# Performance work log

Measured on AMD Instinct MI355X. Metric: run time of the kernel, lower is better.

The kernel has to match this reference:

```python
import jax, jax.numpy as jnp
import numpy as np

NUM_NODES = 10000
NUM_EDGES = 640000
IN_CH = 128
HID = 128
OUT_CH = 1


def setup_inputs() -> dict:
    key = jax.random.key(0)
    ks = jax.random.split(key, 12)
    x = jax.random.normal(ks[0], (NUM_NODES, IN_CH), dtype=jnp.float32)
    edge_index = jax.random.randint(ks[1], (2, NUM_EDGES), 0, NUM_NODES, dtype=jnp.int64)
    edge_weight = jax.random.uniform(ks[2], (NUM_EDGES,), dtype=jnp.float32)
    s1 = 1.0 / np.sqrt(IN_CH)
    s2 = 1.0 / np.sqrt(HID)
    W1 = jax.random.uniform(ks[3], (HID, IN_CH), minval=-s1, maxval=s1, dtype=jnp.float32)
    b1 = jnp.zeros((HID,), dtype=jnp.float32)
    W2 = jax.random.uniform(ks[4], (HID, HID), minval=-s2, maxval=s2, dtype=jnp.float32)
    b2 = jnp.zeros((HID,), dtype=jnp.float32)
    sc = 1.0 / np.sqrt(HID * 3)
    conv_w = jax.random.uniform(ks[5], (HID, HID, 3), minval=-sc, maxval=sc, dtype=jnp.float32)
    conv_b = jax.random.uniform(ks[6], (HID,), minval=-sc, maxval=sc, dtype=jnp.float32)
    fc_w = jax.random.uniform(ks[7], (OUT_CH, HID), minval=-s2, maxval=s2, dtype=jnp.float32)
    fc_b = jax.random.uniform(ks[8], (OUT_CH,), minval=-s2, maxval=s2, dtype=jnp.float32)
    return {"x": x, "edge_index": edge_index, "edge_weight": edge_weight,
            "W1": W1, "b1": b1, "W2": W2, "b2": b2,
            "conv_w": conv_w, "conv_b": conv_b, "fc_w": fc_w, "fc_b": fc_b}


def _gcn_conv(x, row, col, norm, W, b):
    # PyG GCNConv: linear (no bias in lin), normalized scatter-add, then bias
    xw = x @ W.T                                   # [N, out]
    msg = xw[row] * norm[:, None]                  # gather + edge scale [E, out]
    out = jax.ops.segment_sum(msg, col, num_segments=NUM_NODES)
    return out + b


def reference(x, edge_index, edge_weight, W1, b1, W2, b2, conv_w, conv_b, fc_w, fc_b):
    # gcn_norm with self-loops (fill_value=1.0)
    loop = jnp.arange(NUM_NODES, dtype=edge_index.dtype)
    row = jnp.concatenate([edge_index[0], loop])
    col = jnp.concatenate([edge_index[1], loop])
    w = jnp.concatenate([edge_weight, jnp.ones((NUM_NODES,), dtype=edge_weight.dtype)])
    deg = jax.ops.segment_sum(w, col, num_segments=NUM_NODES)
    dinv = jnp.where(deg > 0, jax.lax.rsqrt(deg), 0.0)
    norm = dinv[row] * w * dinv[col]

    h = jax.nn.relu(_gcn_conv(x, row, col, norm, W1, b1))
    # dropout is identity in eval mode
    h = jax.nn.relu(_gcn_conv(h, row, col, norm, W2, b2))

    # temporal conv1d over node axis: [N,H] -> [1,H,N]
    hc = h.T[None, :, :]
    hc = jax.lax.conv_general_dilated(hc, conv_w, window_strides=(1,),
                                      padding='SAME',
                                      dimension_numbers=('NCH', 'OIH', 'NCH'))
    hc = hc + conv_b[None, :, None]
    h = hc[0].T                                    # [N, H]

    return (h @ fc_w.T + fc_b).squeeze()           # [N]
```

## Files before the change

kernel.cpp:

```cpp
#include <hip/hip_runtime.h>
#include <hip/hip_bf16.h>

#define N_NODES 10000
#define N_EDGES 640000
#define CH 128
#define NB 128
#define EPB (N_EDGES / NB)
#define NCHUNK 40

__global__ __launch_bounds__(256) void hist_kernel(const int* __restrict__ ei,
                                                   const float* __restrict__ ew,
                                                   int* __restrict__ hist,
                                                   float* __restrict__ dhist) {
    __shared__ int h[N_NODES];
    __shared__ float hf[N_NODES];
    int b = blockIdx.x, t = threadIdx.x;
    for (int i = t; i < N_NODES; i += 256) { h[i] = 0; hf[i] = 0.0f; }
    __syncthreads();
    int e0 = b * EPB;
    for (int i = t; i < EPB; i += 256) {
        int c = ei[N_EDGES + e0 + i];
        float w = ew[e0 + i];
        atomicAdd(&h[c], 1);
        atomicAdd(&hf[c], w);
    }
    __syncthreads();
    for (int i = t; i < N_NODES; i += 256) {
        hist[b * N_NODES + i] = h[i];
        dhist[b * N_NODES + i] = hf[i];
    }
}

__global__ __launch_bounds__(256) void reduce_kernel(const int* __restrict__ hist,
        const float* __restrict__ dhist, int* __restrict__ tot,
        float* __restrict__ dinv, int* __restrict__ csum,
        const float* __restrict__ conv_w, const float* __restrict__ conv_b,
        const float* __restrict__ fc_w, const float* __restrict__ fc_b,
        float* __restrict__ vbuf, float* __restrict__ c0) {
    int blk = blockIdx.x, t = threadIdx.x;
    if (blk == NCHUNK) {
        for (int i = t; i <= 384; i += 256) {
            if (i < 384) {
                float s = 0.0f;
                for (int o = 0; o < CH; ++o) s += fc_w[o] * conv_w[o * 384 + i];
                vbuf[i] = s;
            } else {
                float s = fc_b[0];
                for (int o = 0; o < CH; ++o) s += fc_w[o] * conv_b[o];
                *c0 = s;
            }
        }
        return;
    }
    int n = blk * 256 + t;
    int c = 0;
    if (n < N_NODES) {
        float d = 0.0f;
        #pragma unroll 4
        for (int b = 0; b < NB; ++b) {
            c += hist[b * N_NODES + n];
            d += dhist[b * N_NODES + n];
        }
        tot[n] = c;
        dinv[n] = rsqrtf(d + 1.0f);
    }
    __shared__ int wred[4];
    int lane = t & 63, wave = t >> 6;
    int s = c;
    #pragma unroll
    for (int off = 32; off > 0; off >>= 1) s += __shfl_down(s, off, 64);
    if (lane == 0) wred[wave] = s;
    __syncthreads();
    if (t == 0) csum[blk] = wred[0] + wred[1] + wred[2] + wred[3];
}

__global__ __launch_bounds__(256) void bofs_kernel(int* __restrict__ hist,
        const int* __restrict__ tot, const int* __restrict__ csum,
        int* __restrict__ offs) {
    __shared__ int lds_csum[NCHUNK];
    __shared__ int wsum[4];
    int blk = blockIdx.x, t = threadIdx.x;
    if (t < NCHUNK) lds_csum[t] = csum[t];
    __syncthreads();
    int base = 0;
    for (int i = 0; i < blk; ++i) base += lds_csum[i];
    int n = blk * 256 + t;
    int v = (n < N_NODES) ? tot[n] : 0;
    int lane = t & 63, wave = t >> 6;
    int s = v;
    #pragma unroll
    for (int off = 1; off < 64; off <<= 1) {
        int u = __shfl_up(s, off, 64);
        if (lane >= off) s += u;
    }
    if (lane == 63) wsum[wave] = s;
    __syncthreads();
    int wbase = 0;
    for (int i = 0; i < wave; ++i) wbase += wsum[i];
    if (n < N_NODES) {
        int run = base + wbase + s - v;
        offs[n] = run;
        for (int b = 0; b < NB; ++b) {
            int h = hist[b * N_NODES + n];
            hist[b * N_NODES + n] = run;
            run += h;
        }
    }
}

__global__ __launch_bounds__(256) void scatter_kernel(const int* __restrict__ ei,
        const float* __restrict__ ew, const float* __restrict__ dinv,
        const int* __restrict__ bofs, int2* __restrict__ erec) {
    __shared__ int cur[N_NODES];
    __shared__ float di[N_NODES];
    int b = blockIdx.x, t = threadIdx.x;
    for (int i = t; i < N_NODES; i += 256) {
        cur[i] = bofs[b * N_NODES + i];
        di[i] = dinv[i];
    }
    __syncthreads();
    int e0 = b * EPB;
    for (int i = t; i < EPB; i += 256) {
        int e = e0 + i;
        int r = ei[e];
        int c = ei[N_EDGES + e];
        int p = atomicAdd(&cur[c], 1);
        float v = di[r] * ew[e] * di[c];
        erec[p] = make_int2(r, __float_as_int(v));
    }
}

__global__ __launch_bounds__(256) void gemm128_kernel(const float* __restrict__ A,
                                                      const float* __restrict__ W,
                                                      float* __restrict__ out, int M) {
    __shared__ float As[32][68];
    __shared__ float Ws[32][132];
    int tid = threadIdx.x;
    int tx = tid & 31;
    int ty = tid >> 5;
    int row0 = blockIdx.x * 64;
    float acc[8][4] = {};
    for (int k0 = 0; k0 < 128; k0 += 32) {
        #pragma unroll
        for (int i = 0; i < 8; ++i) {
            int idx = tid + i * 256;
            int r = idx >> 5, k = idx & 31;
            int gr = row0 + r;
            As[k][r] = (gr < M) ? A[gr * CH + k0 + k] : 0.0f;
        }
        #pragma unroll
        for (int i = 0; i < 16; ++i) {
            int idx = tid + i * 256;
            int o = idx >> 5, k = idx & 31;
            Ws[k][o] = W[o * CH + k0 + k];
        }
        __syncthreads();
        #pragma unroll
        for (int kk = 0; kk < 32; ++kk) {
            float a[8], w[4];
            #pragma unroll
            for (int j = 0; j < 8; ++j) a[j] = As[kk][ty * 8 + j];
            #pragma unroll
            for (int c = 0; c < 4; ++c) w[c] = Ws[kk][tx * 4 + c];
            #pragma unroll
            for (int j = 0; j < 8; ++j)
                #pragma unroll
                for (int c = 0; c < 4; ++c)
                    acc[j][c] += a[j] * w[c];
        }
        __syncthreads();
    }
    #pragma unroll
    for (int j = 0; j < 8; ++j) {
        int gr = row0 + ty * 8 + j;
        if (gr < M) {
            float4 v = make_float4(acc[j][0], acc[j][1], acc[j][2], acc[j][3]);
            *reinterpret_cast<float4*>(&out[gr * CH + tx * 4]) = v;
        }
    }
}

__global__ __launch_bounds__(256) void agg_kernel(const float4* __restrict__ xw4,
        const int2* __restrict__ erec, const int* __restrict__ offs,
        const int* __restrict__ cnt, const float* __restrict__ dinv,
        const float4* __restrict__ bias4, float4* __restrict__ out4) {
    int l = threadIdx.x & 31;
    int g = threadIdx.x >> 5;
    int n = blockIdx.x * 8 + g;
    float d = dinv[n];
    float dd = d * d;
    float4 self = xw4[n * 32 + l];
    float4 acc = make_float4(dd * self.x, dd * self.y, dd * self.z, dd * self.w);
    int start = offs[n];
    int num = cnt[n];
    int i = 0;
    for (; i + 8 <= num; i += 8) {
        int2 r[8];
        #pragma unroll
        for (int j = 0; j < 8; ++j) r[j] = erec[start + i + j];
        float4 f[8];
        #pragma unroll
        for (int j = 0; j < 8; ++j) f[j] = xw4[r[j].x * 32 + l];
        #pragma unroll
        for (int j = 0; j < 8; ++j) {
            float v = __int_as_float(r[j].y);
            acc.x += v * f[j].x; acc.y += v * f[j].y;
            acc.z += v * f[j].z; acc.w += v * f[j].w;
        }
    }
    for (; i < num; ++i) {
        int2 r = erec[start + i];
        float4 f = xw4[r.x * 32 + l];
        float v = __int_as_float(r.y);
        acc.x += v * f.x; acc.y += v * f.y; acc.z += v * f.z; acc.w += v * f.w;
    }
    float4 bb = bias4[l];
    acc.x = fmaxf(acc.x + bb.x, 0.0f);
    acc.y = fmaxf(acc.y + bb.y, 0.0f);
    acc.z = fmaxf(acc.z + bb.z, 0.0f);
    acc.w = fmaxf(acc.w + bb.w, 0.0f);
    out4[n * 32 + l] = acc;
}

__global__ __launch_bounds__(128) void convfc_kernel(const float* __restrict__ h,
        const float* __restrict__ v, const float* __restrict__ c0,
        float* __restrict__ out, int N) {
    int n = blockIdx.x;
    int t = threadIdx.x;
    float p = 0.0f;
    if (n > 0)     p += h[(n - 1) * CH + t] * v[t * 3 + 0];
    p += h[n * CH + t] * v[t * 3 + 1];
    if (n < N - 1) p += h[(n + 1) * CH + t] * v[t * 3 + 2];
    #pragma unroll
    for (int off = 32; off > 0; off >>= 1) p += __shfl_down(p, off, 64);
    __shared__ float red[2];
    if ((t & 63) == 0) red[t >> 6] = p;
    __syncthreads();
    if (t == 0) out[n] = red[0] + red[1] + *c0;
}

extern "C" void kernel_launch(void* const* d_in, const int* in_sizes, int n_in,
                              void* d_out, int out_size, void* d_ws, size_t ws_size,
                              hipStream_t stream) {
    const float* x       = (const float*)d_in[0];
    const int*   ei      = (const int*)d_in[1];
    const float* ew      = (const float*)d_in[2];
    const float* W1      = (const float*)d_in[3];
    const float* b1      = (const float*)d_in[4];
    const float* W2      = (const float*)d_in[5];
    const float* b2      = (const float*)d_in[6];
    const float* conv_w  = (const float*)d_in[7];
    const float* conv_b  = (const float*)d_in[8];
    const float* fc_w    = (const float*)d_in[9];
    const float* fc_b    = (const float*)d_in[10];
    float* out = (float*)d_out;

    float* bufA   = (float*)d_ws;
    float* bufB   = bufA + N_NODES * CH;
    int2*  erec   = (int2*)(bufB + N_NODES * CH);
    int*   hist   = (int*)bufA;
    float* dhist  = (float*)erec;
    int*   tot    = (int*)(erec + N_EDGES);
    int*   offs   = tot + N_NODES;
    float* dinv   = (float*)(offs + N_NODES);
    float* vbuf   = dinv + N_NODES;
    float* c0     = vbuf + 384;
    int*   csum   = (int*)(c0 + 1);

    hist_kernel<<<NB, 256, 0, stream>>>(ei, ew, hist, dhist);
    reduce_kernel<<<NCHUNK + 1, 256, 0, stream>>>(hist, dhist, tot, dinv, csum,
                                                  conv_w, conv_b, fc_w, fc_b, vbuf, c0);
    bofs_kernel<<<NCHUNK, 256, 0, stream>>>(hist, tot, csum, offs);
    scatter_kernel<<<NB, 256, 0, stream>>>(ei, ew, dinv, hist, erec);

    const int gemm_grid = (N_NODES + 63) / 64;
    gemm128_kernel<<<gemm_grid, 256, 0, stream>>>(x, W1, bufA, N_NODES);
    agg_kernel<<<N_NODES / 8, 256, 0, stream>>>((const float4*)bufA, erec, offs, tot,
                                                dinv, (const float4*)b1, (float4*)bufB);
    gemm128_kernel<<<gemm_grid, 256, 0, stream>>>(bufB, W2, bufA, N_NODES);
    agg_kernel<<<N_NODES / 8, 256, 0, stream>>>((const float4*)bufA, erec, offs, tot,
                                                dinv, (const float4*)b2, (float4*)bufB);
    convfc_kernel<<<N_NODES, 128, 0, stream>>>(bufB, vbuf, c0, out, N_NODES);
}
```

Baseline: 229.2 us.

## Replace per-block histogram CSR build with global atomics and single-block scan

The CSR construction changes from 128 per-block LDS histograms, a reduce pass, and a per-block offset pass to global atomic counting of degrees, one 1024-thread scan kernel, and a scatter that uses global atomic cursors. This removes the large hist/dhist round-trips and one kernel launch, but puts contention on global atomics over 10000 nodes. The conv+fc kernel now handles four nodes per block with one wave each, so the LDS reduction and barrier go away. Edge order within a bucket becomes nondeterministic, which can change float summation order.

```diff
diff --git a/kernel.cpp b/kernel.cpp
--- a/kernel.cpp
+++ b/kernel.cpp
@@ -4,130 +4,74 @@
 #define N_NODES 10000
 #define N_EDGES 640000
 #define CH 128
-#define NB 128
-#define EPB (N_EDGES / NB)
-#define NCHUNK 40
-
-__global__ __launch_bounds__(256) void hist_kernel(const int* __restrict__ ei,
-                                                   const float* __restrict__ ew,
-                                                   int* __restrict__ hist,
-                                                   float* __restrict__ dhist) {
-    __shared__ int h[N_NODES];
-    __shared__ float hf[N_NODES];
-    int b = blockIdx.x, t = threadIdx.x;
-    for (int i = t; i < N_NODES; i += 256) { h[i] = 0; hf[i] = 0.0f; }
-    __syncthreads();
-    int e0 = b * EPB;
-    for (int i = t; i < EPB; i += 256) {
-        int c = ei[N_EDGES + e0 + i];
-        float w = ew[e0 + i];
-        atomicAdd(&h[c], 1);
-        atomicAdd(&hf[c], w);
-    }
-    __syncthreads();
-    for (int i = t; i < N_NODES; i += 256) {
-        hist[b * N_NODES + i] = h[i];
-        dhist[b * N_NODES + i] = hf[i];
-    }
-}
-
-__global__ __launch_bounds__(256) void reduce_kernel(const int* __restrict__ hist,
-        const float* __restrict__ dhist, int* __restrict__ tot,
-        float* __restrict__ dinv, int* __restrict__ csum,
+
+__global__ __launch_bounds__(256) void cnt_kernel(const int* __restrict__ ei,
+                                                  const float* __restrict__ ew,
+                                                  int* __restrict__ tot,
+                                                  float* __restrict__ deg) {
+    int e = blockIdx.x * 256 + threadIdx.x;
+    int c = ei[N_EDGES + e];
+    float w = ew[e];
+    atomicAdd(&tot[c], 1);
+    atomicAdd(&deg[c], w);
+}
+
+__global__ __launch_bounds__(1024) void scan_kernel(const int* __restrict__ tot,
+        const float* __restrict__ deg, int* __restrict__ offs, int* __restrict__ cur,
+        float* __restrict__ dinv,
         const float* __restrict__ conv_w, const float* __restrict__ conv_b,
         const float* __restrict__ fc_w, const float* __restrict__ fc_b,
         float* __restrict__ vbuf, float* __restrict__ c0) {
-    int blk = blockIdx.x, t = threadIdx.x;
-    if (blk == NCHUNK) {
-        for (int i = t; i <= 384; i += 256) {
-            if (i < 384) {
-                float s = 0.0f;
-                for (int o = 0; o < CH; ++o) s += fc_w[o] * conv_w[o * 384 + i];
-                vbuf[i] = s;
-            } else {
-                float s = fc_b[0];
-                for (int o = 0; o < CH; ++o) s += fc_w[o] * conv_b[o];
-                *c0 = s;
-            }
-        }
-        return;
-    }
-    int n = blk * 256 + t;
-    int c = 0;
-    if (n < N_NODES) {
-        float d = 0.0f;
-        #pragma unroll 4
-        for (int b = 0; b < NB; ++b) {
-            c += hist[b * N_NODES + n];
-            d += dhist[b * N_NODES + n];
-        }
-        tot[n] = c;
-        dinv[n] = rsqrtf(d + 1.0f);
-    }
-    __shared__ int wred[4];
+    __shared__ int lt[10240];
+    __shared__ int wsum[16];
+    int t = threadIdx.x;
+    for (int i = t; i < 10240; i += 1024) lt[i] = (i < N_NODES) ? tot[i] : 0;
+    for (int i = t; i < N_NODES; i += 1024) dinv[i] = rsqrtf(deg[i] + 1.0f);
+    if (t < 384) {
+        float s = 0.0f;
+        for (int o = 0; o < CH; ++o) s += fc_w[o] * conv_w[o * 384 + t];
+        vbuf[t] = s;
+    } else if (t == 384) {
+        float s = fc_b[0];
+        for (int o = 0; o < CH; ++o) s += fc_w[o] * conv_b[o];
+        *c0 = s;
+    }
+    __syncthreads();
+    int base = t * 10;
+    int loc[10]; int s = 0;
+    #pragma unroll
+    for (int j = 0; j < 10; ++j) { loc[j] = s; s += lt[base + j]; }
     int lane = t & 63, wave = t >> 6;
-    int s = c;
-    #pragma unroll
-    for (int off = 32; off > 0; off >>= 1) s += __shfl_down(s, off, 64);
-    if (lane == 0) wred[wave] = s;
-    __syncthreads();
-    if (t == 0) csum[blk] = wred[0] + wred[1] + wred[2] + wred[3];
-}
-
-__global__ __launch_bounds__(256) void bofs_kernel(int* __restrict__ hist,
-        const int* __restrict__ tot, const int* __restrict__ csum,
-        int* __restrict__ offs) {
-    __shared__ int lds_csum[NCHUNK];
-    __shared__ int wsum[4];
-    int blk = blockIdx.x, t = threadIdx.x;
-    if (t < NCHUNK) lds_csum[t] = csum[t];
-    __syncthreads();
-    int base = 0;
-    for (int i = 0; i < blk; ++i) base += lds_csum[i];
-    int n = blk * 256 + t;
-    int v = (n < N_NODES) ? tot[n] : 0;
-    int lane = t & 63, wave = t >> 6;
-    int s = v;
+    int inc = s;
     #pragma unroll
     for (int off = 1; off < 64; off <<= 1) {
-        int u = __shfl_up(s, off, 64);
-        if (lane >= off) s += u;
-    }
-    if (lane == 63) wsum[wave] = s;
+        int u = __shfl_up(inc, off, 64);
+        if (lane >= off) inc += u;
+    }
+    if (lane == 63) wsum[wave] = inc;
     __syncthreads();
     int wbase = 0;
     for (int i = 0; i < wave; ++i) wbase += wsum[i];
-    if (n < N_NODES) {
-        int run = base + wbase + s - v;
-        offs[n] = run;
-        for (int b = 0; b < NB; ++b) {
-            int h = hist[b * N_NODES + n];
-            hist[b * N_NODES + n] = run;
-            run += h;
-        }
+    int ex = wbase + inc - s;
+    #pragma unroll
+    for (int j = 0; j < 10; ++j) lt[base + j] = ex + loc[j];
+    __syncthreads();
+    for (int i = t; i < N_NODES; i += 1024) {
+        int v = lt[i];
+        offs[i] = v;
+        cur[i] = v;
     }
 }
 
 __global__ __launch_bounds__(256) void scatter_kernel(const int* __restrict__ ei,
         const float* __restrict__ ew, const float* __restrict__ dinv,
-        const int* __restrict__ bofs, int2* __restrict__ erec) {
-    __shared__ int cur[N_NODES];
-    __shared__ float di[N_NODES];
-    int b = blockIdx.x, t = threadIdx.x;
-    for (int i = t; i < N_NODES; i += 256) {
-        cur[i] = bofs[b * N_NODES + i];
-        di[i] = dinv[i];
-    }
-    __syncthreads();
-    int e0 = b * EPB;
-    for (int i = t; i < EPB; i += 256) {
-        int e = e0 + i;
-        int r = ei[e];
-        int c = ei[N_EDGES + e];
-        int p = atomicAdd(&cur[c], 1);
-        float v = di[r] * ew[e] * di[c];
-        erec[p] = make_int2(r, __float_as_int(v));
-    }
+        int* __restrict__ cur, int2* __restrict__ erec) {
+    int e = blockIdx.x * 256 + threadIdx.x;
+    int r = ei[e];
+    int c = ei[N_EDGES + e];
+    float v = dinv[r] * ew[e] * dinv[c];
+    int p = atomicAdd(&cur[c], 1);
+    erec[p] = make_int2(r, __float_as_int(v));
 }
 
 __global__ __launch_bounds__(256) void gemm128_kernel(const float* __restrict__ A,
@@ -222,21 +166,21 @@
     out4[n * 32 + l] = acc;
 }
 
-__global__ __launch_bounds__(128) void convfc_kernel(const float* __restrict__ h,
+__global__ __launch_bounds__(256) void convfc_kernel(const float* __restrict__ h,
         const float* __restrict__ v, const float* __restrict__ c0,
         float* __restrict__ out, int N) {
-    int n = blockIdx.x;
-    int t = threadIdx.x;
-    float p = 0.0f;
-    if (n > 0)     p += h[(n - 1) * CH + t] * v[t * 3 + 0];
-    p += h[n * CH + t] * v[t * 3 + 1];
-    if (n < N - 1) p += h[(n + 1) * CH + t] * v[t * 3 + 2];
+    int n = blockIdx.x * 4 + (threadIdx.x >> 6);
+    int l = threadIdx.x & 63;
+    if (n >= N) return;
+    const float* hn = h + n * CH;
+    float v0a = v[l * 3 + 0],        v1a = v[l * 3 + 1],        v2a = v[l * 3 + 2];
+    float v0b = v[(l + 64) * 3 + 0], v1b = v[(l + 64) * 3 + 1], v2b = v[(l + 64) * 3 + 2];
+    float p = hn[l] * v1a + hn[l + 64] * v1b;
+    if (n > 0)     p += hn[l - CH] * v0a + hn[l + 64 - CH] * v0b;
+    if (n < N - 1) p += hn[l + CH] * v2a + hn[l + 64 + CH] * v2b;
     #pragma unroll
     for (int off = 32; off > 0; off >>= 1) p += __shfl_down(p, off, 64);
-    __shared__ float red[2];
-    if ((t & 63) == 0) red[t >> 6] = p;
-    __syncthreads();
-    if (t == 0) out[n] = red[0] + red[1] + *c0;
+    if (l == 0) out[n] = p + *c0;
 }
 
 extern "C" void kernel_launch(void* const* d_in, const int* in_sizes, int n_in,
@@ -258,20 +202,19 @@
     float* bufA   = (float*)d_ws;
     float* bufB   = bufA + N_NODES * CH;
     int2*  erec   = (int2*)(bufB + N_NODES * CH);
-    int*   hist   = (int*)bufA;
-    float* dhist  = (float*)erec;
     int*   tot    = (int*)(erec + N_EDGES);
-    int*   offs   = tot + N_NODES;
-    float* dinv   = (float*)(offs + N_NODES);
+    float* deg    = (float*)(tot + N_NODES);
+    int*   offs   = (int*)(deg + N_NODES);
+    int*   cur    = offs + N_NODES;
+    float* dinv   = (float*)(cur + N_NODES);
     float* vbuf   = dinv + N_NODES;
     float* c0     = vbuf + 384;
-    int*   csum   = (int*)(c0 + 1);
-
-    hist_kernel<<<NB, 256, 0, stream>>>(ei, ew, hist, dhist);
-    reduce_kernel<<<NCHUNK + 1, 256, 0, stream>>>(hist, dhist, tot, dinv, csum,
-                                                  conv_w, conv_b, fc_w, fc_b, vbuf, c0);
-    bofs_kernel<<<NCHUNK, 256, 0, stream>>>(hist, tot, csum, offs);
-    scatter_kernel<<<NB, 256, 0, stream>>>(ei, ew, dinv, hist, erec);
+
+    hipMemsetAsync(tot, 0, 2 * N_NODES * sizeof(int), stream);
+    cnt_kernel<<<N_EDGES / 256, 256, 0, stream>>>(ei, ew, tot, deg);
+    scan_kernel<<<1, 1024, 0, stream>>>(tot, deg, offs, cur, dinv,
+                                        conv_w, conv_b, fc_w, fc_b, vbuf, c0);
+    scatter_kernel<<<N_EDGES / 256, 256, 0, stream>>>(ei, ew, dinv, cur, erec);
 
     const int gemm_grid = (N_NODES + 63) / 64;
     gemm128_kernel<<<gemm_grid, 256, 0, stream>>>(x, W1, bufA, N_NODES);
@@ -280,5 +223,5 @@
     gemm128_kernel<<<gemm_grid, 256, 0, stream>>>(bufB, W2, bufA, N_NODES);
     agg_kernel<<<N_NODES / 8, 256, 0, stream>>>((const float4*)bufA, erec, offs, tot,
                                                 dinv, (const float4*)b2, (float4*)bufB);
-    convfc_kernel<<<N_NODES, 128, 0, stream>>>(bufB, vbuf, c0, out, N_NODES);
-}
+    convfc_kernel<<<(N_NODES + 3) / 4, 256, 0, stream>>>(bufB, vbuf, c0, out, N_NODES);
+}
```

After: 303.0 us. 1.32x slower.
